# Kernel tuning notes

Hardware: AMD Instinct MI355X
Metric: run time of the kernel (lower is better)

## Reference

```python
import jax, jax.numpy as jnp
import numpy as np

B, T, I, H = 8192, 1024, 3, 4


def setup_inputs() -> dict:
    key = jax.random.key(0)
    k_x, k_wi, k_wh, k_bi, k_bh = jax.random.split(key, 5)
    s = 1.0 / np.sqrt(H)  # PyTorch GRU init scale uniform(-1/sqrt(H), 1/sqrt(H))
    return {
        "x": jax.random.normal(k_x, (B, T, I), dtype=jnp.float32),
        "w_ih": jax.random.uniform(k_wi, (3 * H, I), jnp.float32, -s, s),
        "w_hh": jax.random.uniform(k_wh, (3 * H, H), jnp.float32, -s, s),
        "b_ih": jax.random.uniform(k_bi, (3 * H,), jnp.float32, -s, s),
        "b_hh": jax.random.uniform(k_bh, (3 * H,), jnp.float32, -s, s),
    }


def _gru_forward(x, w_ih, w_hh, b_ih, b_hh):
    # Precompute input projections for all timesteps: [B, T, 3H]
    gi = jnp.einsum('bti,gi->btg', x, w_ih) + b_ih
    gi = jnp.swapaxes(gi, 0, 1)  # [T, B, 3H] for scan over time
    h0 = jnp.zeros((x.shape[0], H), dtype=x.dtype)

    def step(h, gi_t):
        gh = h @ w_hh.T + b_hh                      # [B, 3H]
        i_r, i_z, i_n = jnp.split(gi_t, 3, axis=-1)
        h_r, h_z, h_n = jnp.split(gh, 3, axis=-1)
        r = jax.nn.sigmoid(i_r + h_r)
        z = jax.nn.sigmoid(i_z + h_z)
        n = jnp.tanh(i_n + r * h_n)
        h_new = (1.0 - z) * n + z * h
        return h_new, h_new

    h_last, outs = jax.lax.scan(step, h0, gi)
    out = jnp.swapaxes(outs, 0, 1)  # [B, T, H] (batch_first)
    h_n = h_last[None]              # [1, B, H] (num_layers*dirs, B, H)
    return out, h_n


def reference(x, w_ih, w_hh, b_ih, b_hh):
    return _gru_forward(x, w_ih, w_hh, b_ih, b_hh)
```

## Files before the change

### kernel.cpp

```cpp
#include <hip/hip_runtime.h>


#define TC 16
#define GI_TS 192
#define OS_STRIDE 68

template<int CTRL>
__device__ __forceinline__ float dpp_rot(float v) {
    int i = __builtin_bit_cast(int, v);
    int r = __builtin_amdgcn_mov_dpp(i, CTRL, 0xf, 0xf, true);
    return __builtin_bit_cast(float, r);
}
__device__ __forceinline__ float vrcp(float x)  { return __builtin_amdgcn_rcpf(x); }
__device__ __forceinline__ float vexp2(float x) { return __builtin_amdgcn_exp2f(x); }

__global__ __launch_bounds__(128) void gru_kernel(
    const float* __restrict__ x,
    const float* __restrict__ w_ih,
    const float* __restrict__ w_hh,
    const float* __restrict__ b_ih,
    const float* __restrict__ b_hh,
    float* __restrict__ out)
{
    __shared__ float gi_s[2][TC * GI_TS];
    __shared__ float out_s[2][16 * OS_STRIDE];

    const int tid = threadIdx.x;
    const int b0  = blockIdx.x * 16;

    const float NL2E = -1.4426950408889634f;
    const float P2   =  2.8853900817779268f;

    if (tid < 64) {
        const int q = tid >> 2;
        const int j = tid & 3;

        float whr[4], whz[4], whn[4];
        #pragma unroll
        for (int m = 0; m < 4; ++m) {
            int k = (j + m) & 3;
            whr[m] = NL2E * w_hh[j * 4 + k];
            whz[m] = NL2E * w_hh[(4 + j) * 4 + k];
            whn[m] = P2   * w_hh[(8 + j) * 4 + k];
        }
        const float bhn = P2 * b_hh[8 + j];

        float h = 0.0f;
        __syncthreads();

        for (int c = 0; c < 64; ++c) {
            const float* gb = &gi_s[c & 1][q * 12 + j];
            float*       os = &out_s[c & 1][q * OS_STRIDE];

            float sr[TC], sz[TC], sn[TC];
            #pragma unroll
            for (int t = 0; t < TC; ++t) {
                sr[t] = gb[t * GI_TS];
                sz[t] = gb[t * GI_TS + 4];
                sn[t] = gb[t * GI_TS + 8];
            }

            #pragma unroll
            for (int t = 0; t < TC; ++t) {
                float h1 = dpp_rot<0x39>(h);
                float h2 = dpp_rot<0x4E>(h);
                float h3 = dpp_rot<0x93>(h);
                float gr = fmaf(whr[0], h, whr[1] * h1) + fmaf(whr[2], h2, whr[3] * h3);
                float gz = fmaf(whz[0], h, whz[1] * h1) + fmaf(whz[2], h2, whz[3] * h3);
                float gn = fmaf(whn[0], h, whn[1] * h1) + fmaf(whn[2], h2, fmaf(whn[3], h3, bhn));

                float r = vrcp(1.0f + vexp2(sr[t] + gr));
                float z = vrcp(1.0f + vexp2(sz[t] + gz));
                float omz   = 1.0f - z;
                float szh   = fmaf(z, h, omz);
                float m2omz = -2.0f * omz;
                float u = vrcp(1.0f + vexp2(fmaf(r, gn, sn[t])));
                h = fmaf(m2omz, u, szh);

                os[t * 4 + j] = h;
            }
            __syncthreads();
        }
        out[33554432LL + (long long)(b0 + q) * 4 + j] = h;

    } else {
        const int hl = tid - 64;
        const int bb = hl >> 2;
        const int s  = hl & 3;

        float wr[4][3], wz[4][3], wn[4][3];
        float cbr[4], cbz[4], cbn[4];
        #pragma unroll
        for (int jj = 0; jj < 4; ++jj) {
            #pragma unroll
            for (int k = 0; k < 3; ++k) {
                wr[jj][k] = NL2E * w_ih[jj * 3 + k];
                wz[jj][k] = NL2E * w_ih[(4 + jj) * 3 + k];
                wn[jj][k] = P2   * w_ih[(8 + jj) * 3 + k];
            }
            cbr[jj] = NL2E * (b_ih[jj]     + b_hh[jj]);
            cbz[jj] = NL2E * (b_ih[4 + jj] + b_hh[4 + jj]);
            cbn[jj] = P2   * b_ih[8 + jj];
        }

        const long long xbase = (long long)(b0 + bb) * 3072;

        auto compute_gi = [&](int cc, float* buf) {
            #pragma unroll
            for (int k = 0; k < 4; ++k) {
                int tl = k * 4 + s;
                const float* xp = x + xbase + (long long)(cc * TC + tl) * 3;
                float x0 = xp[0], x1 = xp[1], x2 = xp[2];
                float* gp = &buf[tl * GI_TS + bb * 12];
                #pragma unroll
                for (int jj = 0; jj < 4; ++jj) {
                    gp[jj]     = fmaf(wr[jj][0], x0, fmaf(wr[jj][1], x1, fmaf(wr[jj][2], x2, cbr[jj])));
                    gp[4 + jj] = fmaf(wz[jj][0], x0, fmaf(wz[jj][1], x1, fmaf(wz[jj][2], x2, cbz[jj])));
                    gp[8 + jj] = fmaf(wn[jj][0], x0, fmaf(wn[jj][1], x1, fmaf(wn[jj][2], x2, cbn[jj])));
                }
            }
        };
        auto flush_out = [&](int cc, const float* buf) {
            #pragma unroll
            for (int u = 0; u < 4; ++u) {
                int f   = u * 64 + hl;
                int bbf = f >> 4;
                int idx = f & 15;
                float4 v = *(const float4*)&buf[bbf * OS_STRIDE + idx * 4];
                *(float4*)(out + (long long)(b0 + bbf) * 4096 + cc * 64 + idx * 4) = v;
            }
        };

        compute_gi(0, gi_s[0]);
        __syncthreads();

        for (int c = 0; c < 64; ++c) {
            if (c < 63) compute_gi(c + 1, gi_s[(c + 1) & 1]);
            if (c > 0)  flush_out(c - 1, out_s[(c - 1) & 1]);
            __syncthreads();
        }
        flush_out(63, out_s[1]);
    }
}

extern "C" void kernel_launch(void* const* d_in, const int* in_sizes, int n_in,
                              void* d_out, int out_size, void* d_ws, size_t ws_size,
                              hipStream_t stream) {
    const float* x    = (const float*)d_in[0];
    const float* w_ih = (const float*)d_in[1];
    const float* w_hh = (const float*)d_in[2];
    const float* b_ih = (const float*)d_in[3];
    const float* b_hh = (const float*)d_in[4];
    float* out = (float*)d_out;

    dim3 grid(512), block(128);
    gru_kernel<<<grid, block, 0, stream>>>(x, w_ih, w_hh, b_ih, b_hh, out);
}
```

Before: 268.5 us.

## Interleave two independent GRU batch chains per recurrent thread, halve grid

Each recurrent lane now advances two batch rows (A and B) at once, so the two independent dependency chains can hide each other's exp/rcp and DPP latency. The block covers 32 batch rows instead of 16, the grid shrinks to 256 blocks, and time chunks drop to 8 steps over 128 iterations. The gi and out shared-memory layouts are reorganised into gate-major and time-major strides to match. The cost is half as many blocks to spread over the CUs and twice as many barriers per sequence.

After: 328.4 us. 22.3% more time.

```diff
diff --git a/kernel.cpp b/kernel.cpp
--- a/kernel.cpp
+++ b/kernel.cpp
@@ -1,9 +1,10 @@
 #include <hip/hip_runtime.h>
 
 
-#define TC 16
-#define GI_TS 192
-#define OS_STRIDE 68
+#define TC 8
+#define GI_T 480
+#define GI_G 160
+#define OS_T 132
 
 template<int CTRL>
 __device__ __forceinline__ float dpp_rot(float v) {
@@ -22,18 +23,18 @@
     const float* __restrict__ b_hh,
     float* __restrict__ out)
 {
-    __shared__ float gi_s[2][TC * GI_TS];
-    __shared__ float out_s[2][16 * OS_STRIDE];
+    __shared__ float gi_s[2][TC * GI_T];
+    __shared__ __align__(16) float out_s[2][TC * OS_T];
 
     const int tid = threadIdx.x;
-    const int b0  = blockIdx.x * 16;
+    const int b0  = blockIdx.x * 32;
 
     const float NL2E = -1.4426950408889634f;
     const float P2   =  2.8853900817779268f;
 
     if (tid < 64) {
-        const int q = tid >> 2;
-        const int j = tid & 3;
+        const int qd = tid >> 2;
+        const int j  = tid & 3;
 
         float whr[4], whz[4], whn[4];
         #pragma unroll
@@ -45,48 +46,64 @@
         }
         const float bhn = P2 * b_hh[8 + j];
 
-        float h = 0.0f;
+        float hA = 0.0f, hB = 0.0f;
         __syncthreads();
 
-        for (int c = 0; c < 64; ++c) {
-            const float* gb = &gi_s[c & 1][q * 12 + j];
-            float*       os = &out_s[c & 1][q * OS_STRIDE];
+        for (int c = 0; c < 128; ++c) {
+            const float* g = &gi_s[c & 1][qd * 5 + j];
+            float*      os = &out_s[c & 1][(qd << 2) + j];
 
-            float sr[TC], sz[TC], sn[TC];
+            float srA[TC], szA[TC], snA[TC], srB[TC], szB[TC], snB[TC];
             #pragma unroll
             for (int t = 0; t < TC; ++t) {
-                sr[t] = gb[t * GI_TS];
-                sz[t] = gb[t * GI_TS + 4];
-                sn[t] = gb[t * GI_TS + 8];
+                const float* gt = g + t * GI_T;
+                srA[t] = gt[0];          srB[t] = gt[80];
+                szA[t] = gt[GI_G];       szB[t] = gt[GI_G + 80];
+                snA[t] = gt[2 * GI_G];   snB[t] = gt[2 * GI_G + 80];
             }
 
             #pragma unroll
             for (int t = 0; t < TC; ++t) {
-                float h1 = dpp_rot<0x39>(h);
-                float h2 = dpp_rot<0x4E>(h);
-                float h3 = dpp_rot<0x93>(h);
-                float gr = fmaf(whr[0], h, whr[1] * h1) + fmaf(whr[2], h2, whr[3] * h3);
-                float gz = fmaf(whz[0], h, whz[1] * h1) + fmaf(whz[2], h2, whz[3] * h3);
-                float gn = fmaf(whn[0], h, whn[1] * h1) + fmaf(whn[2], h2, fmaf(whn[3], h3, bhn));
+                float hA1 = dpp_rot<0x39>(hA);
+                float hA2 = dpp_rot<0x4E>(hA);
+                float hA3 = dpp_rot<0x93>(hA);
+                float hB1 = dpp_rot<0x39>(hB);
+                float hB2 = dpp_rot<0x4E>(hB);
+                float hB3 = dpp_rot<0x93>(hB);
 
-                float r = vrcp(1.0f + vexp2(sr[t] + gr));
-                float z = vrcp(1.0f + vexp2(sz[t] + gz));
-                float omz   = 1.0f - z;
-                float szh   = fmaf(z, h, omz);
-                float m2omz = -2.0f * omz;
-                float u = vrcp(1.0f + vexp2(fmaf(r, gn, sn[t])));
-                h = fmaf(m2omz, u, szh);
+                float aRA = fmaf(whr[3], hA3, fmaf(whr[2], hA2, fmaf(whr[1], hA1, fmaf(whr[0], hA, srA[t]))));
+                float aRB = fmaf(whr[3], hB3, fmaf(whr[2], hB2, fmaf(whr[1], hB1, fmaf(whr[0], hB, srB[t]))));
+                float aZA = fmaf(whz[3], hA3, fmaf(whz[2], hA2, fmaf(whz[1], hA1, fmaf(whz[0], hA, szA[t]))));
+                float aZB = fmaf(whz[3], hB3, fmaf(whz[2], hB2, fmaf(whz[1], hB1, fmaf(whz[0], hB, szB[t]))));
+                float gNA = fmaf(whn[3], hA3, fmaf(whn[2], hA2, fmaf(whn[1], hA1, fmaf(whn[0], hA, bhn))));
+                float gNB = fmaf(whn[3], hB3, fmaf(whn[2], hB2, fmaf(whn[1], hB1, fmaf(whn[0], hB, bhn))));
 
-                os[t * 4 + j] = h;
+                float rA = vrcp(1.0f + vexp2(aRA));
+                float rB = vrcp(1.0f + vexp2(aRB));
+                float zA = vrcp(1.0f + vexp2(aZA));
+                float zB = vrcp(1.0f + vexp2(aZB));
+
+                float omzA = 1.0f - zA,            omzB = 1.0f - zB;
+                float szhA = fmaf(zA, hA, omzA),   szhB = fmaf(zB, hB, omzB);
+                float m2A  = -2.0f * omzA,         m2B  = -2.0f * omzB;
+
+                float uA = vrcp(1.0f + vexp2(fmaf(rA, gNA, snA[t])));
+                float uB = vrcp(1.0f + vexp2(fmaf(rB, gNB, snB[t])));
+                hA = fmaf(m2A, uA, szhA);
+                hB = fmaf(m2B, uB, szhB);
+
+                os[t * OS_T]      = hA;
+                os[t * OS_T + 64] = hB;
             }
             __syncthreads();
         }
-        out[33554432LL + (long long)(b0 + q) * 4 + j] = h;
+        out[33554432LL + (long long)(b0 + qd) * 4 + j]      = hA;
+        out[33554432LL + (long long)(b0 + 16 + qd) * 4 + j] = hB;
 
     } else {
         const int hl = tid - 64;
-        const int bb = hl >> 2;
-        const int s  = hl & 3;
+        const int bb = hl >> 1;
+        const int s  = hl & 1;
 
         float wr[4][3], wz[4][3], wn[4][3];
         float cbr[4], cbz[4], cbn[4];
@@ -108,38 +125,38 @@
         auto compute_gi = [&](int cc, float* buf) {
             #pragma unroll
             for (int k = 0; k < 4; ++k) {
-                int tl = k * 4 + s;
+                int tl = k * 2 + s;
                 const float* xp = x + xbase + (long long)(cc * TC + tl) * 3;
                 float x0 = xp[0], x1 = xp[1], x2 = xp[2];
-                float* gp = &buf[tl * GI_TS + bb * 12];
+                float* gp = &buf[tl * GI_T + bb * 5];
                 #pragma unroll
                 for (int jj = 0; jj < 4; ++jj) {
-                    gp[jj]     = fmaf(wr[jj][0], x0, fmaf(wr[jj][1], x1, fmaf(wr[jj][2], x2, cbr[jj])));
-                    gp[4 + jj] = fmaf(wz[jj][0], x0, fmaf(wz[jj][1], x1, fmaf(wz[jj][2], x2, cbz[jj])));
-                    gp[8 + jj] = fmaf(wn[jj][0], x0, fmaf(wn[jj][1], x1, fmaf(wn[jj][2], x2, cbn[jj])));
+                    gp[jj]             = fmaf(wr[jj][0], x0, fmaf(wr[jj][1], x1, fmaf(wr[jj][2], x2, cbr[jj])));
+                    gp[GI_G + jj]      = fmaf(wz[jj][0], x0, fmaf(wz[jj][1], x1, fmaf(wz[jj][2], x2, cbz[jj])));
+                    gp[2 * GI_G + jj]  = fmaf(wn[jj][0], x0, fmaf(wn[jj][1], x1, fmaf(wn[jj][2], x2, cbn[jj])));
                 }
             }
         };
         auto flush_out = [&](int cc, const float* buf) {
             #pragma unroll
             for (int u = 0; u < 4; ++u) {
-                int f   = u * 64 + hl;
-                int bbf = f >> 4;
-                int idx = f & 15;
-                float4 v = *(const float4*)&buf[bbf * OS_STRIDE + idx * 4];
-                *(float4*)(out + (long long)(b0 + bbf) * 4096 + cc * 64 + idx * 4) = v;
+                int f  = u * 64 + hl;
+                int fb = f >> 3;
+                int ft = f & 7;
+                float4 v = *(const float4*)&buf[ft * OS_T + fb * 4];
+                *(float4*)(out + (long long)(b0 + fb) * 4096 + (long long)(cc * TC + ft) * 4) = v;
             }
         };
 
         compute_gi(0, gi_s[0]);
         __syncthreads();
 
-        for (int c = 0; c < 64; ++c) {
-            if (c < 63) compute_gi(c + 1, gi_s[(c + 1) & 1]);
-            if (c > 0)  flush_out(c - 1, out_s[(c - 1) & 1]);
+        for (int c = 0; c < 128; ++c) {
+            if (c < 127) compute_gi(c + 1, gi_s[(c + 1) & 1]);
+            if (c > 0)   flush_out(c - 1, out_s[(c - 1) & 1]);
             __syncthreads();
         }
-        flush_out(63, out_s[1]);
+        flush_out(127, out_s[1]);
     }
 }
 
@@ -153,6 +170,6 @@
     const float* b_hh = (const float*)d_in[4];
     float* out = (float*)d_out;
 
-    dim3 grid(512), block(128);
+    dim3 grid(256), block(128);
     gru_kernel<<<grid, block, 0, stream>>>(x, w_ih, w_hh, b_ih, b_hh, out);
 }
```

## Pack many recurrent waves per block with vectorized prefetching producer waves

Applied to the files above, without the earlier changes.

Restructures the kernel into 768-thread blocks covering 128 batch rows, with 8 waves running the GRU recurrence and 4 producer waves computing input projections and flushing outputs. Producers load x with float4 vectors and prefetch two chunks ahead in registers, and the time chunk is halved to 8 steps. The goal is better latency hiding and wider memory access, but it launches only 64 blocks and doubles the number of block-wide barriers.

Result: slower. 352.5 us (+31.3%).

```diff
diff --git a/kernel.cpp b/kernel.cpp
--- a/kernel.cpp
+++ b/kernel.cpp
@@ -1,9 +1,9 @@
 #include <hip/hip_runtime.h>
 
 
-#define TC 16
-#define GI_TS 192
-#define OS_STRIDE 68
+#define TC 8
+#define NB 128
+#define OS_W 36
 
 template<int CTRL>
 __device__ __forceinline__ float dpp_rot(float v) {
@@ -14,7 +14,7 @@
 __device__ __forceinline__ float vrcp(float x)  { return __builtin_amdgcn_rcpf(x); }
 __device__ __forceinline__ float vexp2(float x) { return __builtin_amdgcn_exp2f(x); }
 
-__global__ __launch_bounds__(128) void gru_kernel(
+__global__ __launch_bounds__(768) void gru_kernel(
     const float* __restrict__ x,
     const float* __restrict__ w_ih,
     const float* __restrict__ w_hh,
@@ -22,18 +22,22 @@
     const float* __restrict__ b_hh,
     float* __restrict__ out)
 {
-    __shared__ float gi_s[2][TC * GI_TS];
-    __shared__ float out_s[2][16 * OS_STRIDE];
+    __shared__ __align__(16) float gi_s[2][TC][NB][12];
+    __shared__ __align__(16) float out_s[2][NB][OS_W];
 
-    const int tid = threadIdx.x;
-    const int b0  = blockIdx.x * 16;
+    const int tid  = threadIdx.x;
+    const int wid  = tid >> 6;
+    const int lane = tid & 63;
+    const int b0   = blockIdx.x * NB;
 
     const float NL2E = -1.4426950408889634f;
     const float P2   =  2.8853900817779268f;
 
-    if (tid < 64) {
-        const int q = tid >> 2;
-        const int j = tid & 3;
+    if ((wid % 3) != 2) {
+        const int r  = wid - (wid + 1) / 3;
+        const int qd = lane >> 2;
+        const int j  = lane & 3;
+        const int bl = r * 16 + qd;
 
         float whr[4], whz[4], whn[4];
         #pragma unroll
@@ -48,16 +52,17 @@
         float h = 0.0f;
         __syncthreads();
 
-        for (int c = 0; c < 64; ++c) {
-            const float* gb = &gi_s[c & 1][q * 12 + j];
-            float*       os = &out_s[c & 1][q * OS_STRIDE];
+        for (int c = 0; c < 128; ++c) {
+            const float* gb = &gi_s[c & 1][0][bl][j];
+            float*       os = &out_s[c & 1][bl][0];
 
             float sr[TC], sz[TC], sn[TC];
             #pragma unroll
             for (int t = 0; t < TC; ++t) {
-                sr[t] = gb[t * GI_TS];
-                sz[t] = gb[t * GI_TS + 4];
-                sn[t] = gb[t * GI_TS + 8];
+                const float* gt = gb + t * (NB * 12);
+                sr[t] = gt[0];
+                sz[t] = gt[4];
+                sn[t] = gt[8];
             }
 
             #pragma unroll
@@ -69,24 +74,25 @@
                 float gz = fmaf(whz[0], h, whz[1] * h1) + fmaf(whz[2], h2, whz[3] * h3);
                 float gn = fmaf(whn[0], h, whn[1] * h1) + fmaf(whn[2], h2, fmaf(whn[3], h3, bhn));
 
-                float r = vrcp(1.0f + vexp2(sr[t] + gr));
-                float z = vrcp(1.0f + vexp2(sz[t] + gz));
+                float rr = vrcp(1.0f + vexp2(sr[t] + gr));
+                float z  = vrcp(1.0f + vexp2(sz[t] + gz));
                 float omz   = 1.0f - z;
                 float szh   = fmaf(z, h, omz);
                 float m2omz = -2.0f * omz;
-                float u = vrcp(1.0f + vexp2(fmaf(r, gn, sn[t])));
+                float u = vrcp(1.0f + vexp2(fmaf(rr, gn, sn[t])));
                 h = fmaf(m2omz, u, szh);
 
                 os[t * 4 + j] = h;
             }
             __syncthreads();
         }
-        out[33554432LL + (long long)(b0 + q) * 4 + j] = h;
+        out[33554432LL + (long long)(b0 + bl) * 4 + j] = h;
 
     } else {
-        const int hl = tid - 64;
-        const int bb = hl >> 2;
-        const int s  = hl & 3;
+        const int hw   = wid / 3;
+        const int cell = hw * 64 + lane;
+        const int bb   = cell >> 1;
+        const int half = cell & 1;
 
         float wr[4][3], wz[4][3], wn[4][3];
         float cbr[4], cbz[4], cbn[4];
@@ -103,43 +109,60 @@
             cbn[jj] = P2   * b_ih[8 + jj];
         }
 
-        const long long xbase = (long long)(b0 + bb) * 3072;
+        const float* xp0 = x + (long long)(b0 + bb) * 3072 + half * 12;
 
-        auto compute_gi = [&](int cc, float* buf) {
+        auto compute_gi = [&](int cc, float4 a, float4 b, float4 e, int buf) {
+            float xs[12] = { a.x, a.y, a.z, a.w, b.x, b.y, b.z, b.w, e.x, e.y, e.z, e.w };
             #pragma unroll
-            for (int k = 0; k < 4; ++k) {
-                int tl = k * 4 + s;
-                const float* xp = x + xbase + (long long)(cc * TC + tl) * 3;
-                float x0 = xp[0], x1 = xp[1], x2 = xp[2];
-                float* gp = &buf[tl * GI_TS + bb * 12];
+            for (int dt = 0; dt < 4; ++dt) {
+                float x0 = xs[dt * 3], x1 = xs[dt * 3 + 1], x2 = xs[dt * 3 + 2];
+                float g[12];
                 #pragma unroll
                 for (int jj = 0; jj < 4; ++jj) {
-                    gp[jj]     = fmaf(wr[jj][0], x0, fmaf(wr[jj][1], x1, fmaf(wr[jj][2], x2, cbr[jj])));
-                    gp[4 + jj] = fmaf(wz[jj][0], x0, fmaf(wz[jj][1], x1, fmaf(wz[jj][2], x2, cbz[jj])));
-                    gp[8 + jj] = fmaf(wn[jj][0], x0, fmaf(wn[jj][1], x1, fmaf(wn[jj][2], x2, cbn[jj])));
+                    g[jj]     = fmaf(wr[jj][0], x0, fmaf(wr[jj][1], x1, fmaf(wr[jj][2], x2, cbr[jj])));
+                    g[4 + jj] = fmaf(wz[jj][0], x0, fmaf(wz[jj][1], x1, fmaf(wz[jj][2], x2, cbz[jj])));
+                    g[8 + jj] = fmaf(wn[jj][0], x0, fmaf(wn[jj][1], x1, fmaf(wn[jj][2], x2, cbn[jj])));
                 }
+                float4* gp = (float4*)&gi_s[buf][half * 4 + dt][bb][0];
+                gp[0] = make_float4(g[0], g[1], g[2],  g[3]);
+                gp[1] = make_float4(g[4], g[5], g[6],  g[7]);
+                gp[2] = make_float4(g[8], g[9], g[10], g[11]);
             }
         };
-        auto flush_out = [&](int cc, const float* buf) {
+        auto flush_out = [&](int cc, int buf) {
             #pragma unroll
             for (int u = 0; u < 4; ++u) {
-                int f   = u * 64 + hl;
-                int bbf = f >> 4;
-                int idx = f & 15;
-                float4 v = *(const float4*)&buf[bbf * OS_STRIDE + idx * 4];
-                *(float4*)(out + (long long)(b0 + bbf) * 4096 + cc * 64 + idx * 4) = v;
+                int f  = u * 256 + cell;
+                int fb = f >> 3;
+                int ft = f & 7;
+                float4 v = *(const float4*)&out_s[buf][fb][ft * 4];
+                *(float4*)(out + (long long)(b0 + fb) * 4096 + (long long)(cc * TC + ft) * 4) = v;
             }
         };
 
-        compute_gi(0, gi_s[0]);
+        float4 nx0 = *(const float4*)(xp0 + 0);
+        float4 nx1 = *(const float4*)(xp0 + 4);
+        float4 nx2 = *(const float4*)(xp0 + 8);
+        compute_gi(0, nx0, nx1, nx2, 0);
+        nx0 = *(const float4*)(xp0 + 24);
+        nx1 = *(const float4*)(xp0 + 28);
+        nx2 = *(const float4*)(xp0 + 32);
         __syncthreads();
 
-        for (int c = 0; c < 64; ++c) {
-            if (c < 63) compute_gi(c + 1, gi_s[(c + 1) & 1]);
-            if (c > 0)  flush_out(c - 1, out_s[(c - 1) & 1]);
+        for (int c = 0; c < 128; ++c) {
+            float4 t0, t1, t2;
+            if (c < 126) {
+                const float* xp = xp0 + (long long)(c + 2) * 24;
+                t0 = *(const float4*)(xp + 0);
+                t1 = *(const float4*)(xp + 4);
+                t2 = *(const float4*)(xp + 8);
+            }
+            if (c < 127) compute_gi(c + 1, nx0, nx1, nx2, (c + 1) & 1);
+            if (c > 0)   flush_out(c - 1, (c - 1) & 1);
+            if (c < 126) { nx0 = t0; nx1 = t1; nx2 = t2; }
             __syncthreads();
         }
-        flush_out(63, out_s[1]);
+        flush_out(127, 1);
     }
 }
 
@@ -153,6 +176,6 @@
     const float* b_hh = (const float*)d_in[4];
     float* out = (float*)d_out;
 
-    dim3 grid(512), block(128);
+    dim3 grid(64), block(768);
     gru_kernel<<<grid, block, 0, stream>>>(x, w_ih, w_hh, b_ih, b_hh, out);
 }
```

## Triple-buffer gate inputs, prefetch next chunk into registers, polynomial sigmoid

Applied to the files above, without the earlier changes.

The gate-input shared buffer grows from two to three slots, so the producer warp can compute two chunks ahead. The recurrence warp now loads the next chunk's gate inputs into a second register set before it runs the current chunk. This is meant to hide LDS load latency behind the serial recurrence. Separately, the r and n gates swap the exp+reciprocal sigmoid for exp2(-|a|) followed by a polynomial and a sign select, dropping one rcp from the critical path. The costs are doubled register use for the staged arrays and approximation error in those gates.

Measured after the change: 283.6 us. 5.6% more time.

```diff
diff --git a/kernel.cpp b/kernel.cpp
--- a/kernel.cpp
+++ b/kernel.cpp
@@ -22,7 +22,7 @@
     const float* __restrict__ b_hh,
     float* __restrict__ out)
 {
-    __shared__ float gi_s[2][TC * GI_TS];
+    __shared__ float gi_s[3][TC * GI_TS];
     __shared__ float out_s[2][16 * OS_STRIDE];
 
     const int tid = threadIdx.x;
@@ -46,39 +46,65 @@
         const float bhn = P2 * b_hh[8 + j];
 
         float h = 0.0f;
-        __syncthreads();
+        float srA[TC], szA[TC], snA[TC], srB[TC], szB[TC], snB[TC];
 
-        for (int c = 0; c < 64; ++c) {
-            const float* gb = &gi_s[c & 1][q * 12 + j];
-            float*       os = &out_s[c & 1][q * OS_STRIDE];
-
-            float sr[TC], sz[TC], sn[TC];
+        auto stage = [&](int c, float* SR, float* SZ, float* SN) {
+            const float* gb = &gi_s[c % 3][q * 12 + j];
             #pragma unroll
             for (int t = 0; t < TC; ++t) {
-                sr[t] = gb[t * GI_TS];
-                sz[t] = gb[t * GI_TS + 4];
-                sn[t] = gb[t * GI_TS + 8];
+                SR[t] = gb[t * GI_TS];
+                SZ[t] = gb[t * GI_TS + 4];
+                SN[t] = gb[t * GI_TS + 8];
             }
+        };
 
+        auto run16 = [&](int c, const float* SR, const float* SZ, const float* SN) {
+            float* os = &out_s[c & 1][q * OS_STRIDE];
             #pragma unroll
             for (int t = 0; t < TC; ++t) {
                 float h1 = dpp_rot<0x39>(h);
                 float h2 = dpp_rot<0x4E>(h);
                 float h3 = dpp_rot<0x93>(h);
-                float gr = fmaf(whr[0], h, whr[1] * h1) + fmaf(whr[2], h2, whr[3] * h3);
-                float gz = fmaf(whz[0], h, whz[1] * h1) + fmaf(whz[2], h2, whz[3] * h3);
-                float gn = fmaf(whn[0], h, whn[1] * h1) + fmaf(whn[2], h2, fmaf(whn[3], h3, bhn));
 
-                float r = vrcp(1.0f + vexp2(sr[t] + gr));
-                float z = vrcp(1.0f + vexp2(sz[t] + gz));
+                float aR = (fmaf(whr[0], h, SR[t]) + whr[1] * h1)
+                         + fmaf(whr[2], h2, whr[3] * h3);
+                float aZ = (fmaf(whz[0], h, SZ[t]) + whz[1] * h1)
+                         + fmaf(whz[2], h2, whz[3] * h3);
+                float gn = fmaf(whn[0], h, whn[1] * h1)
+                         + fmaf(whn[2], h2, fmaf(whn[3], h3, bhn));
+
+                float Vr = vexp2(-__builtin_fabsf(aR));
+                float gr = fmaf(Vr, fmaf(Vr, fmaf(Vr, fmaf(Vr,
+                               0.156856f, -0.542276f), 0.871966f), -0.986113f), 0.999751f);
+                float r  = (aR > 0.0f) ? Vr * gr : gr;
+
+                float z = vrcp(1.0f + vexp2(aZ));
                 float omz   = 1.0f - z;
                 float szh   = fmaf(z, h, omz);
                 float m2omz = -2.0f * omz;
-                float u = vrcp(1.0f + vexp2(fmaf(r, gn, sn[t])));
+
+                float e  = fmaf(r, gn, SN[t]);
+                float Vn = vexp2(-__builtin_fabsf(e));
+                float gu = fmaf(Vn, fmaf(Vn, fmaf(Vn, fmaf(Vn, fmaf(Vn,
+                               -0.10764288f, 0.4259632f), -0.7777448f),
+                               0.956062f), -0.996625f), 0.99996124f);
+                float u  = (e > 0.0f) ? Vn * gu : gu;
+
                 h = fmaf(m2omz, u, szh);
 
                 os[t * 4 + j] = h;
             }
+        };
+
+        __syncthreads();
+        stage(0, srA, szA, snA);
+
+        for (int c = 0; c < 64; c += 2) {
+            stage(c + 1, srB, szB, snB);
+            run16(c, srA, szA, snA);
+            __syncthreads();
+            if (c + 2 < 64) stage(c + 2, srA, szA, snA);
+            run16(c + 1, srB, szB, snB);
             __syncthreads();
         }
         out[33554432LL + (long long)(b0 + q) * 4 + j] = h;
@@ -132,10 +158,11 @@
         };
 
         compute_gi(0, gi_s[0]);
+        compute_gi(1, gi_s[1]);
         __syncthreads();
 
         for (int c = 0; c < 64; ++c) {
-            if (c < 63) compute_gi(c + 1, gi_s[(c + 1) & 1]);
+            if (c < 62) compute_gi(c + 2, gi_s[(c + 2) % 3]);
             if (c > 0)  flush_out(c - 1, out_s[(c - 1) & 1]);
             __syncthreads();
         }
```
